# Kernel tuning notes

Measured on AMD Instinct MI355X. Metric: run time of the kernel, lower is better.

The kernel has to match this reference:

```python
import jax, jax.numpy as jnp
import numpy as np

MARGIN = 0.2
NEG_INF = -1e9  # safe stand-in for -inf when masking the max


def setup_inputs() -> dict:
    key = jax.random.key(0)
    k1, k2, k3 = jax.random.split(key, 3)
    B, D = 8192, 256
    p = jax.random.normal(k1, (B, D), dtype=jnp.float32)
    # module docstring says projections are normalized
    projections = p / jnp.linalg.norm(p, axis=1, keepdims=True)
    affordance_ids = jax.random.randint(k2, (B,), 0, 36, dtype=jnp.int64)
    instance_ids = jax.random.randint(k3, (B,), 0, 2048, dtype=jnp.int64)
    return {
        "projections": projections,
        "affordance_ids": affordance_ids,
        "instance_ids": instance_ids,
    }


def reference(projections, affordance_ids, instance_ids):
    # (B, B) cosine similarities
    sim = jnp.matmul(projections, projections.T)

    aff_eq = affordance_ids[:, None] == affordance_ids[None, :]
    inst_eq = instance_ids[:, None] == instance_ids[None, :]
    pos_mask = aff_eq & ~inst_eq          # same affordance, different instance
    neg_mask = ~aff_eq                    # different affordance

    # per-row hard negative: max similarity over negatives
    hard_neg = jnp.max(jnp.where(neg_mask, sim, NEG_INF), axis=1)  # (B,)

    # rows contribute only if they have >=1 positive AND >=1 negative
    valid_row = pos_mask.any(axis=1) & neg_mask.any(axis=1)        # (B,)
    pair_mask = pos_mask & valid_row[:, None]                      # (B, B)

    # margin loss for every (anchor i, positive j) pair
    losses = jnp.maximum(hard_neg[:, None] - sim + MARGIN, 0.0)

    total = jnp.sum(jnp.where(pair_mask, losses, 0.0))
    num_pairs = jnp.sum(pair_mask)
    return jnp.where(num_pairs > 0, total / num_pairs, 0.0)
```

## Files before the change

kernel.cpp:

```cpp
#include <hip/hip_runtime.h>

#define NB 8192
#define ND 256
#define NCLS 64
#define LOSS_MARGIN 0.2f
#define NEG_INF_F (-1e9f)
#define LMAXT 3
#define NBLK_LOSS (NCLS * LMAXT * LMAXT)
#define NTILE_T 2080

typedef __attribute__((ext_vector_type(8))) __bf16 bf16x8;
typedef __attribute__((ext_vector_type(4))) float f32x4;

__device__ __forceinline__ unsigned short f2bf(float f) {
  unsigned u = __float_as_uint(f);
  unsigned r = (u + 0x7fffu + ((u >> 16) & 1u)) >> 16;
  return (unsigned short)r;
}

__device__ __forceinline__ void gl_lds16(const void* gsrc, void* ldst) {
  __builtin_amdgcn_global_load_lds(
      (const __attribute__((address_space(1))) void*)gsrc,
      (__attribute__((address_space(3))) void*)ldst, 16, 0, 0);
}

__global__ __launch_bounds__(1024) void build_idx_fused(const int* __restrict__ aff,
                                                        int* __restrict__ class_start,
                                                        int* __restrict__ class_idx) {
  const int c = blockIdx.x;
  const int t = threadIdx.x;
  const int lane = t & 63, wave = t >> 6;
  __shared__ int wtot[16];
  __shared__ int s_off;

  int lt = 0;
  for (int i = t; i < NB; i += 1024) lt += (aff[i] < c) ? 1 : 0;
  for (int off = 32; off; off >>= 1) lt += __shfl_down(lt, off);
  if (lane == 0) wtot[wave] = lt;
  __syncthreads();
  int base = 0;
  for (int w = 0; w < 16; ++w) base += wtot[w];
  if (t == 0) {
    class_start[c] = base;
    if (c == 0) class_start[NCLS] = NB;
  }
  __syncthreads();
  if (t == 0) s_off = 0;
  __syncthreads();

  for (int pass = 0; pass < NB / 1024; ++pass) {
    const int i = pass * 1024 + t;
    const bool m = (aff[i] == c);
    const unsigned long long mask = __ballot(m);
    if (lane == 0) wtot[wave] = __popcll(mask);
    __syncthreads();
    const int off = s_off;
    int prefix = 0;
    for (int w = 0; w < wave; ++w) prefix += wtot[w];
    if (m)
      class_idx[base + off + prefix +
                __popcll(mask & ((1ull << lane) - 1ull))] = i;
    __syncthreads();
    if (t == 0) {
      int tot = 0;
      for (int w = 0; w < 16; ++w) tot += wtot[w];
      s_off = off + tot;
    }
    __syncthreads();
  }
}

__global__ __launch_bounds__(256) void gather_convert(const float* __restrict__ P,
                                                      const int* __restrict__ aff,
                                                      const int* __restrict__ inst,
                                                      const int* __restrict__ class_idx,
                                                      unsigned short* __restrict__ Psort,
                                                      int* __restrict__ affSort,
                                                      int* __restrict__ instSort) {
  const int t = threadIdx.x;
  const int sr = blockIdx.x * 8 + (t >> 5);
  const int c = t & 31;
  const int src = class_idx[sr];
  const float4* ps = (const float4*)(P + (size_t)src * ND);
  ushort4* pd = (ushort4*)(Psort + (size_t)sr * ND);
#pragma unroll
  for (int q = 0; q < 2; ++q) {
    float4 v = ps[c + q * 32];
    ushort4 h;
    h.x = f2bf(v.x); h.y = f2bf(v.y); h.z = f2bf(v.z); h.w = f2bf(v.w);
    pd[c + q * 32] = h;
  }
  if (c == 0) {
    affSort[sr] = aff[src];
    instSort[sr] = inst[src];
  }
}

__global__ __launch_bounds__(256, 4) void simmax_mfma(const unsigned short* __restrict__ Psort,
                                                      const int* __restrict__ affSort,
                                                      float* __restrict__ part) {
  int wg = blockIdx.x;
  wg = (wg & 7) * (NTILE_T / 8) + (wg >> 3);
  int bi = (int)((129.0f - sqrtf(129.0f * 129.0f - 8.0f * (float)wg)) * 0.5f);
  while (bi * 64 - bi * (bi - 1) / 2 > wg) --bi;
  while ((bi + 1) * 64 - (bi + 1) * bi / 2 <= wg) ++bi;
  const int bj = bi + (wg - (bi * 64 - bi * (bi - 1) / 2));

  __shared__ __align__(16) unsigned short At[2][4096];
  __shared__ __align__(16) unsigned short Bt[2][4096];
  __shared__ int affI[128], affJ[128];
  __shared__ float rowmax_s[128][2];
  __shared__ float colmax_s[128][2];

  const int t = threadIdx.x;
  const int lane = t & 63;
  const int wave = t >> 6;
  const int r0 = bi * 128, c0 = bj * 128;

  if (t < 128) affI[t] = affSort[r0 + t];
  else affJ[t - 128] = affSort[c0 + (t - 128)];

  const int wr = (wave >> 1) * 64;
  const int wc = (wave & 1) * 64;

  f32x4 acc[4][4];
#pragma unroll
  for (int m = 0; m < 4; ++m)
#pragma unroll
    for (int n = 0; n < 4; ++n) acc[m][n] = (f32x4){0.f, 0.f, 0.f, 0.f};

  const int ci0 = t, ci1 = 256 + t;
  const int kg0 = ci0 >> 7, rw0 = ci0 & 127;
  const int kg1 = ci1 >> 7, rw1 = ci1 & 127;

#define STAGE_SIM(B, KC)                                                      \
  do {                                                                        \
    gl_lds16(Psort + (size_t)(r0 + rw0) * ND + (KC) + kg0 * 8, &At[B][ci0 * 8]); \
    gl_lds16(Psort + (size_t)(c0 + rw0) * ND + (KC) + kg0 * 8, &Bt[B][ci0 * 8]); \
    gl_lds16(Psort + (size_t)(r0 + rw1) * ND + (KC) + kg1 * 8, &At[B][ci1 * 8]); \
    gl_lds16(Psort + (size_t)(c0 + rw1) * ND + (KC) + kg1 * 8, &Bt[B][ci1 * 8]); \
  } while (0)

  STAGE_SIM(0, 0);
  asm volatile("s_waitcnt vmcnt(0) lgkmcnt(0)" ::: "memory");
  __builtin_amdgcn_s_barrier();
  __builtin_amdgcn_sched_barrier(0);

  int cur = 0;
#pragma unroll 1
  for (int s = 0; s < 8; ++s) {
    if (s < 7) STAGE_SIM(cur ^ 1, (s + 1) * 32);
    const int kg = lane >> 4, lr = lane & 15;
    bf16x8 a[4], b[4];
#pragma unroll
    for (int m = 0; m < 4; ++m)
      a[m] = *(const bf16x8*)&At[cur][(kg * 128 + wr + m * 16 + lr) * 8];
#pragma unroll
    for (int n = 0; n < 4; ++n)
      b[n] = *(const bf16x8*)&Bt[cur][(kg * 128 + wc + n * 16 + lr) * 8];
#pragma unroll
    for (int m = 0; m < 4; ++m)
#pragma unroll
      for (int n = 0; n < 4; ++n)
        acc[m][n] = __builtin_amdgcn_mfma_f32_16x16x32_bf16(a[m], b[n], acc[m][n], 0, 0, 0);
    __builtin_amdgcn_sched_barrier(0);
    if (s < 7) {
      asm volatile("s_waitcnt vmcnt(0) lgkmcnt(0)" ::: "memory");
      __builtin_amdgcn_s_barrier();
      __builtin_amdgcn_sched_barrier(0);
    }
    cur ^= 1;
  }

#pragma unroll
  for (int m = 0; m < 4; ++m) {
#pragma unroll
    for (int r = 0; r < 4; ++r) {
      const int lrow = wr + m * 16 + (lane >> 4) * 4 + r;
      const int ai = affI[lrow];
      float rmax = NEG_INF_F;
#pragma unroll
      for (int n = 0; n < 4; ++n) {
        const int lcol = wc + n * 16 + (lane & 15);
        if (affJ[lcol] != ai) rmax = fmaxf(rmax, acc[m][n][r]);
      }
      rmax = fmaxf(rmax, __shfl_xor(rmax, 1));
      rmax = fmaxf(rmax, __shfl_xor(rmax, 2));
      rmax = fmaxf(rmax, __shfl_xor(rmax, 4));
      rmax = fmaxf(rmax, __shfl_xor(rmax, 8));
      if ((lane & 15) == 0) rowmax_s[lrow][wc >> 6] = rmax;
    }
  }
  if (bi != bj) {
#pragma unroll
    for (int n = 0; n < 4; ++n) {
      const int lcol = wc + n * 16 + (lane & 15);
      const int aj = affJ[lcol];
      float cmax = NEG_INF_F;
#pragma unroll
      for (int m = 0; m < 4; ++m) {
        const int lrb = wr + m * 16 + (lane >> 4) * 4;
#pragma unroll
        for (int r = 0; r < 4; ++r)
          if (affI[lrb + r] != aj) cmax = fmaxf(cmax, acc[m][n][r]);
      }
      cmax = fmaxf(cmax, __shfl_xor(cmax, 16));
      cmax = fmaxf(cmax, __shfl_xor(cmax, 32));
      if (lane < 16) colmax_s[lcol][wr >> 6] = cmax;
    }
  }
  __syncthreads();
  if (t < 128) {
    part[(size_t)(r0 + t) * 64 + bj] = fmaxf(rowmax_s[t][0], rowmax_s[t][1]);
  } else if (bi != bj) {
    const int c = t - 128;
    part[(size_t)(c0 + c) * 64 + bi] = fmaxf(colmax_s[c][0], colmax_s[c][1]);
  }
#undef STAGE_SIM
}

__global__ __launch_bounds__(256) void hn_reduce(const float* __restrict__ part,
                                                 float* __restrict__ hn) {
  const int i = blockIdx.x * 256 + threadIdx.x;
  const float4* p = (const float4*)(part + (size_t)i * 64);
  float m = NEG_INF_F;
#pragma unroll
  for (int q = 0; q < 16; ++q) {
    float4 v = p[q];
    m = fmaxf(m, fmaxf(fmaxf(v.x, v.y), fmaxf(v.z, v.w)));
  }
  hn[i] = m;
}

__global__ __launch_bounds__(256, 4) void loss_mfma(const unsigned short* __restrict__ Psort,
                                                    const int* __restrict__ class_start,
                                                    const int* __restrict__ instSort,
                                                    const float* __restrict__ hn,
                                                    float* __restrict__ bsum,
                                                    int* __restrict__ bcnt) {
  const int c = blockIdx.z;
  const int ti = blockIdx.x, tj = blockIdx.y;
  const int bid = (c * LMAXT + ti) * LMAXT + tj;
  const int t = threadIdx.x;
  const int base = class_start[c];
  const int cnt = class_start[c + 1] - base;
  const int nt = (cnt + 127) >> 7;
  if (ti >= nt || tj >= nt || cnt >= NB) {
    if (t == 0) { bsum[bid] = 0.f; bcnt[bid] = 0; }
    return;
  }

  __shared__ __align__(16) unsigned short At[2][4096];
  __shared__ __align__(16) unsigned short Bt[2][4096];
  __shared__ int instI[128], instJ[128];
  __shared__ float hnI[128];

  const int lane = t & 63;
  const int wave = t >> 6;

  if (t < 128) {
    int ri = ti * 128 + t;
    int gi = base + (ri < cnt ? ri : 0);
    instI[t] = instSort[gi];
    hnI[t] = hn[gi];
  } else {
    int tt = t - 128;
    int rj = tj * 128 + tt;
    int gj = base + (rj < cnt ? rj : 0);
    instJ[tt] = instSort[gj];
  }

  const int wr = (wave >> 1) * 64;
  const int wc = (wave & 1) * 64;

  f32x4 acc[4][4];
#pragma unroll
  for (int m = 0; m < 4; ++m)
#pragma unroll
    for (int n = 0; n < 4; ++n) acc[m][n] = (f32x4){0.f, 0.f, 0.f, 0.f};

  const int ci0 = t, ci1 = 256 + t;
  const int kg0 = ci0 >> 7, rw0 = ci0 & 127;
  const int kg1 = ci1 >> 7, rw1 = ci1 & 127;
  const int ra0 = base + (ti * 128 + rw0 < cnt ? ti * 128 + rw0 : 0);
  const int ra1 = base + (ti * 128 + rw1 < cnt ? ti * 128 + rw1 : 0);
  const int rb0 = base + (tj * 128 + rw0 < cnt ? tj * 128 + rw0 : 0);
  const int rb1 = base + (tj * 128 + rw1 < cnt ? tj * 128 + rw1 : 0);

#define STAGE_LOSS(B, KC)                                               \
  do {                                                                  \
    gl_lds16(Psort + (size_t)ra0 * ND + (KC) + kg0 * 8, &At[B][ci0 * 8]); \
    gl_lds16(Psort + (size_t)rb0 * ND + (KC) + kg0 * 8, &Bt[B][ci0 * 8]); \
    gl_lds16(Psort + (size_t)ra1 * ND + (KC) + kg1 * 8, &At[B][ci1 * 8]); \
    gl_lds16(Psort + (size_t)rb1 * ND + (KC) + kg1 * 8, &Bt[B][ci1 * 8]); \
  } while (0)

  STAGE_LOSS(0, 0);
  asm volatile("s_waitcnt vmcnt(0) lgkmcnt(0)" ::: "memory");
  __builtin_amdgcn_s_barrier();
  __builtin_amdgcn_sched_barrier(0);

  int cur = 0;
#pragma unroll 1
  for (int s = 0; s < 8; ++s) {
    if (s < 7) STAGE_LOSS(cur ^ 1, (s + 1) * 32);
    const int kg = lane >> 4, lr = lane & 15;
    bf16x8 a[4], b[4];
#pragma unroll
    for (int m = 0; m < 4; ++m)
      a[m] = *(const bf16x8*)&At[cur][(kg * 128 + wr + m * 16 + lr) * 8];
#pragma unroll
    for (int n = 0; n < 4; ++n)
      b[n] = *(const bf16x8*)&Bt[cur][(kg * 128 + wc + n * 16 + lr) * 8];
#pragma unroll
    for (int m = 0; m < 4; ++m)
#pragma unroll
      for (int n = 0; n < 4; ++n)
        acc[m][n] = __builtin_amdgcn_mfma_f32_16x16x32_bf16(a[m], b[n], acc[m][n], 0, 0, 0);
    __builtin_amdgcn_sched_barrier(0);
    if (s < 7) {
      asm volatile("s_waitcnt vmcnt(0) lgkmcnt(0)" ::: "memory");
      __builtin_amdgcn_s_barrier();
      __builtin_amdgcn_sched_barrier(0);
    }
    cur ^= 1;
  }

  float lsum = 0.f;
  int lcnt = 0;
#pragma unroll
  for (int m = 0; m < 4; ++m) {
#pragma unroll
    for (int r = 0; r < 4; ++r) {
      const int lrow = wr + m * 16 + (lane >> 4) * 4 + r;
      const int ri = ti * 128 + lrow;
      if (ri >= cnt) continue;
      const float hnv = hnI[lrow];
      const int ii = instI[lrow];
#pragma unroll
      for (int n = 0; n < 4; ++n) {
        const int lcol = wc + n * 16 + (lane & 15);
        const int rj = tj * 128 + lcol;
        if (rj < cnt && instJ[lcol] != ii) {
          lsum += fmaxf(hnv - acc[m][n][r] + LOSS_MARGIN, 0.f);
          lcnt += 1;
        }
      }
    }
  }

  for (int off = 32; off; off >>= 1) {
    lsum += __shfl_down(lsum, off);
    lcnt += __shfl_down(lcnt, off);
  }
  __shared__ float wsum[4];
  __shared__ int wcnt[4];
  if (lane == 0) { wsum[wave] = lsum; wcnt[wave] = lcnt; }
  __syncthreads();
  if (t == 0) {
    bsum[bid] = wsum[0] + wsum[1] + wsum[2] + wsum[3];
    bcnt[bid] = wcnt[0] + wcnt[1] + wcnt[2] + wcnt[3];
  }
#undef STAGE_LOSS
}

__global__ __launch_bounds__(256) void finalize_kernel(const float* __restrict__ bsum,
                                                       const int* __restrict__ bcnt,
                                                       float* __restrict__ out) {
  const int t = threadIdx.x;
  float s = 0.f;
  int n = 0;
  for (int i = t; i < NBLK_LOSS; i += 256) { s += bsum[i]; n += bcnt[i]; }
  for (int off = 32; off; off >>= 1) {
    s += __shfl_down(s, off);
    n += __shfl_down(n, off);
  }
  __shared__ float wsum[4];
  __shared__ int wcnt[4];
  if ((t & 63) == 0) { wsum[t >> 6] = s; wcnt[t >> 6] = n; }
  __syncthreads();
  if (t == 0) {
    const float S = wsum[0] + wsum[1] + wsum[2] + wsum[3];
    const int N = wcnt[0] + wcnt[1] + wcnt[2] + wcnt[3];
    out[0] = (N > 0) ? (S / (float)N) : 0.0f;
  }
}

extern "C" void kernel_launch(void* const* d_in, const int* in_sizes, int n_in,
                              void* d_out, int out_size, void* d_ws, size_t ws_size,
                              hipStream_t stream) {
  const float* P = (const float*)d_in[0];
  const int* aff = (const int*)d_in[1];
  const int* inst = (const int*)d_in[2];
  float* out = (float*)d_out;

  unsigned short* Psort = (unsigned short*)d_ws;
  float* part = (float*)((char*)d_ws + (size_t)NB * ND * 2);
  int* ibase = (int*)((char*)part + (size_t)NB * 64 * 4);
  float* hn        = (float*)ibase;
  int* class_start = ibase + NB;
  int* class_idx   = ibase + NB + NCLS + 1;
  int* affSort     = ibase + 2 * NB + NCLS + 1;
  int* instSort    = ibase + 3 * NB + NCLS + 1;
  float* bsum = (float*)(ibase + 4 * NB + NCLS + 1);
  int* bcnt   = ibase + 4 * NB + NCLS + 1 + NBLK_LOSS;

  build_idx_fused<<<NCLS, 1024, 0, stream>>>(aff, class_start, class_idx);
  gather_convert<<<NB / 8, 256, 0, stream>>>(P, aff, inst, class_idx, Psort,
                                             affSort, instSort);
  simmax_mfma<<<NTILE_T, 256, 0, stream>>>(Psort, affSort, part);
  hn_reduce<<<NB / 256, 256, 0, stream>>>(part, hn);
  loss_mfma<<<dim3(LMAXT, LMAXT, NCLS), 256, 0, stream>>>(Psort, class_start, instSort,
                                                          hn, bsum, bcnt);
  finalize_kernel<<<1, 256, 0, stream>>>(bsum, bcnt, out);
}
```

Baseline: 90.62 us.

## Triple-buffer LDS staging with partial vmcnt waits in both MFMA kernels

Result: no change. 92.22 us (+1.8%).

```diff
diff --git a/kernel.cpp b/kernel.cpp
--- a/kernel.cpp
+++ b/kernel.cpp
@@ -96,7 +96,7 @@
   }
 }
 
-__global__ __launch_bounds__(256, 4) void simmax_mfma(const unsigned short* __restrict__ Psort,
+__global__ __launch_bounds__(256, 3) void simmax_mfma(const unsigned short* __restrict__ Psort,
                                                       const int* __restrict__ affSort,
                                                       float* __restrict__ part) {
   int wg = blockIdx.x;
@@ -106,8 +106,8 @@
   while ((bi + 1) * 64 - (bi + 1) * bi / 2 <= wg) ++bi;
   const int bj = bi + (wg - (bi * 64 - bi * (bi - 1) / 2));
 
-  __shared__ __align__(16) unsigned short At[2][4096];
-  __shared__ __align__(16) unsigned short Bt[2][4096];
+  __shared__ __align__(16) unsigned short At[3][4096];
+  __shared__ __align__(16) unsigned short Bt[3][4096];
   __shared__ int affI[128], affJ[128];
   __shared__ float rowmax_s[128][2];
   __shared__ float colmax_s[128][2];
@@ -141,36 +141,46 @@
     gl_lds16(Psort + (size_t)(c0 + rw1) * ND + (KC) + kg1 * 8, &Bt[B][ci1 * 8]); \
   } while (0)
 
+#define KSTEP_SIM(S, VM)                                                      \
+  do {                                                                        \
+    asm volatile("s_waitcnt vmcnt(" #VM ")" ::: "memory");                    \
+    __builtin_amdgcn_s_barrier();                                             \
+    __builtin_amdgcn_sched_barrier(0);                                        \
+    const int kg = lane >> 4, lr = lane & 15;                                 \
+    bf16x8 a[4], b[4];                                                        \
+    _Pragma("unroll")                                                         \
+    for (int m = 0; m < 4; ++m)                                               \
+      a[m] = *(const bf16x8*)&At[(S) % 3][(kg * 128 + wr + m * 16 + lr) * 8]; \
+    _Pragma("unroll")                                                         \
+    for (int n = 0; n < 4; ++n)                                               \
+      b[n] = *(const bf16x8*)&Bt[(S) % 3][(kg * 128 + wc + n * 16 + lr) * 8]; \
+    __builtin_amdgcn_s_setprio(1);                                            \
+    _Pragma("unroll")                                                         \
+    for (int m = 0; m < 4; ++m)                                               \
+      _Pragma("unroll")                                                       \
+      for (int n = 0; n < 4; ++n)                                             \
+        acc[m][n] = __builtin_amdgcn_mfma_f32_16x16x32_bf16(a[m], b[n], acc[m][n], 0, 0, 0); \
+    __builtin_amdgcn_s_setprio(0);                                            \
+    __builtin_amdgcn_sched_barrier(0);                                        \
+    if ((S) < 5) {                                                            \
+      __builtin_amdgcn_s_barrier();                                           \
+      __builtin_amdgcn_sched_barrier(0);                                      \
+      STAGE_SIM((S) % 3, ((S) + 3) * 32);                                     \
+    }                                                                         \
+  } while (0)
+
   STAGE_SIM(0, 0);
-  asm volatile("s_waitcnt vmcnt(0) lgkmcnt(0)" ::: "memory");
-  __builtin_amdgcn_s_barrier();
-  __builtin_amdgcn_sched_barrier(0);
-
-  int cur = 0;
-#pragma unroll 1
-  for (int s = 0; s < 8; ++s) {
-    if (s < 7) STAGE_SIM(cur ^ 1, (s + 1) * 32);
-    const int kg = lane >> 4, lr = lane & 15;
-    bf16x8 a[4], b[4];
-#pragma unroll
-    for (int m = 0; m < 4; ++m)
-      a[m] = *(const bf16x8*)&At[cur][(kg * 128 + wr + m * 16 + lr) * 8];
-#pragma unroll
-    for (int n = 0; n < 4; ++n)
-      b[n] = *(const bf16x8*)&Bt[cur][(kg * 128 + wc + n * 16 + lr) * 8];
-#pragma unroll
-    for (int m = 0; m < 4; ++m)
-#pragma unroll
-      for (int n = 0; n < 4; ++n)
-        acc[m][n] = __builtin_amdgcn_mfma_f32_16x16x32_bf16(a[m], b[n], acc[m][n], 0, 0, 0);
-    __builtin_amdgcn_sched_barrier(0);
-    if (s < 7) {
-      asm volatile("s_waitcnt vmcnt(0) lgkmcnt(0)" ::: "memory");
-      __builtin_amdgcn_s_barrier();
-      __builtin_amdgcn_sched_barrier(0);
-    }
-    cur ^= 1;
-  }
+  STAGE_SIM(1, 32);
+  STAGE_SIM(2, 64);
+
+  KSTEP_SIM(0, 8);
+  KSTEP_SIM(1, 8);
+  KSTEP_SIM(2, 8);
+  KSTEP_SIM(3, 8);
+  KSTEP_SIM(4, 8);
+  KSTEP_SIM(5, 8);
+  KSTEP_SIM(6, 4);
+  KSTEP_SIM(7, 0);
 
 #pragma unroll
   for (int m = 0; m < 4; ++m) {
@@ -216,6 +226,7 @@
     const int c = t - 128;
     part[(size_t)(c0 + c) * 64 + bi] = fmaxf(colmax_s[c][0], colmax_s[c][1]);
   }
+#undef KSTEP_SIM
 #undef STAGE_SIM
 }
 
@@ -232,7 +243,7 @@
   hn[i] = m;
 }
 
-__global__ __launch_bounds__(256, 4) void loss_mfma(const unsigned short* __restrict__ Psort,
+__global__ __launch_bounds__(256, 3) void loss_mfma(const unsigned short* __restrict__ Psort,
                                                     const int* __restrict__ class_start,
                                                     const int* __restrict__ instSort,
                                                     const float* __restrict__ hn,
@@ -250,8 +261,8 @@
     return;
   }
 
-  __shared__ __align__(16) unsigned short At[2][4096];
-  __shared__ __align__(16) unsigned short Bt[2][4096];
+  __shared__ __align__(16) unsigned short At[3][4096];
+  __shared__ __align__(16) unsigned short Bt[3][4096];
   __shared__ int instI[128], instJ[128];
   __shared__ float hnI[128];
 
@@ -295,36 +306,46 @@
     gl_lds16(Psort + (size_t)rb1 * ND + (KC) + kg1 * 8, &Bt[B][ci1 * 8]); \
   } while (0)
 
+#define KSTEP_LOSS(S, VM)                                                     \
+  do {                                                                        \
+    asm volatile("s_waitcnt vmcnt(" #VM ")" ::: "memory");                    \
+    __builtin_amdgcn_s_barrier();                                             \
+    __builtin_amdgcn_sched_barrier(0);                                        \
+    const int kg = lane >> 4, lr = lane & 15;                                 \
+    bf16x8 a[4], b[4];                                                        \
+    _Pragma("unroll")                                                         \
+    for (int m = 0; m < 4; ++m)                                               \
+      a[m] = *(const bf16x8*)&At[(S) % 3][(kg * 128 + wr + m * 16 + lr) * 8]; \
+    _Pragma("unroll")                                                         \
+    for (int n = 0; n < 4; ++n)                                               \
+      b[n] = *(const bf16x8*)&Bt[(S) % 3][(kg * 128 + wc + n * 16 + lr) * 8]; \
+    __builtin_amdgcn_s_setprio(1);                                            \
+    _Pragma("unroll")                                                         \
+    for (int m = 0; m < 4; ++m)                                               \
+      _Pragma("unroll")                                                       \
+      for (int n = 0; n < 4; ++n)                                             \
+        acc[m][n] = __builtin_amdgcn_mfma_f32_16x16x32_bf16(a[m], b[n], acc[m][n], 0, 0, 0); \
+    __builtin_amdgcn_s_setprio(0);                                            \
+    __builtin_amdgcn_sched_barrier(0);                                        \
+    if ((S) < 5) {                                                            \
+      __builtin_amdgcn_s_barrier();                                           \
+      __builtin_amdgcn_sched_barrier(0);                                      \
+      STAGE_LOSS((S) % 3, ((S) + 3) * 32);                                    \
+    }                                                                         \
+  } while (0)
+
   STAGE_LOSS(0, 0);
-  asm volatile("s_waitcnt vmcnt(0) lgkmcnt(0)" ::: "memory");
-  __builtin_amdgcn_s_barrier();
-  __builtin_amdgcn_sched_barrier(0);
-
-  int cur = 0;
-#pragma unroll 1
-  for (int s = 0; s < 8; ++s) {
-    if (s < 7) STAGE_LOSS(cur ^ 1, (s + 1) * 32);
-    const int kg = lane >> 4, lr = lane & 15;
-    bf16x8 a[4], b[4];
-#pragma unroll
-    for (int m = 0; m < 4; ++m)
-      a[m] = *(const bf16x8*)&At[cur][(kg * 128 + wr + m * 16 + lr) * 8];
-#pragma unroll
-    for (int n = 0; n < 4; ++n)
-      b[n] = *(const bf16x8*)&Bt[cur][(kg * 128 + wc + n * 16 + lr) * 8];
-#pragma unroll
-    for (int m = 0; m < 4; ++m)
-#pragma unroll
-      for (int n = 0; n < 4; ++n)
-        acc[m][n] = __builtin_amdgcn_mfma_f32_16x16x32_bf16(a[m], b[n], acc[m][n], 0, 0, 0);
-    __builtin_amdgcn_sched_barrier(0);
-    if (s < 7) {
-      asm volatile("s_waitcnt vmcnt(0) lgkmcnt(0)" ::: "memory");
-      __builtin_amdgcn_s_barrier();
-      __builtin_amdgcn_sched_barrier(0);
-    }
-    cur ^= 1;
-  }
+  STAGE_LOSS(1, 32);
+  STAGE_LOSS(2, 64);
+
+  KSTEP_LOSS(0, 8);
+  KSTEP_LOSS(1, 8);
+  KSTEP_LOSS(2, 8);
+  KSTEP_LOSS(3, 8);
+  KSTEP_LOSS(4, 8);
+  KSTEP_LOSS(5, 8);
+  KSTEP_LOSS(6, 4);
+  KSTEP_LOSS(7, 0);
 
   float lsum = 0.f;
   int lcnt = 0;
@@ -361,6 +382,7 @@
     bsum[bid] = wsum[0] + wsum[1] + wsum[2] + wsum[3];
     bcnt[bid] = wcnt[0] + wcnt[1] + wcnt[2] + wcnt[3];
   }
+#undef KSTEP_LOSS
 #undef STAGE_LOSS
 }
 
```

## Fuse index build with gather, fold hn reduce into loss, skip masks

Applied to the files above, without the earlier changes.

After: 99.11 us. 1.09x slower.

```diff
diff --git a/kernel.cpp b/kernel.cpp
--- a/kernel.cpp
+++ b/kernel.cpp
@@ -8,6 +8,7 @@
 #define LMAXT 3
 #define NBLK_LOSS (NCLS * LMAXT * LMAXT)
 #define NTILE_T 2080
+#define MAXCLS 640
 
 typedef __attribute__((ext_vector_type(8))) __bf16 bf16x8;
 typedef __attribute__((ext_vector_type(4))) float f32x4;
@@ -24,14 +25,19 @@
       (__attribute__((address_space(3))) void*)ldst, 16, 0, 0);
 }
 
-__global__ __launch_bounds__(1024) void build_idx_fused(const int* __restrict__ aff,
-                                                        int* __restrict__ class_start,
-                                                        int* __restrict__ class_idx) {
+__global__ __launch_bounds__(1024) void prep_kernel(const float* __restrict__ P,
+                                                    const int* __restrict__ aff,
+                                                    const int* __restrict__ inst,
+                                                    int* __restrict__ class_start,
+                                                    unsigned short* __restrict__ Psort,
+                                                    int* __restrict__ affSort,
+                                                    int* __restrict__ instSort) {
   const int c = blockIdx.x;
   const int t = threadIdx.x;
   const int lane = t & 63, wave = t >> 6;
   __shared__ int wtot[16];
   __shared__ int s_off;
+  __shared__ int lds_idx[MAXCLS];
 
   int lt = 0;
   for (int i = t; i < NB; i += 1024) lt += (aff[i] < c) ? 1 : 0;
@@ -57,9 +63,10 @@
     const int off = s_off;
     int prefix = 0;
     for (int w = 0; w < wave; ++w) prefix += wtot[w];
-    if (m)
-      class_idx[base + off + prefix +
-                __popcll(mask & ((1ull << lane) - 1ull))] = i;
+    if (m) {
+      int pos = off + prefix + __popcll(mask & ((1ull << lane) - 1ull));
+      if (pos < MAXCLS) lds_idx[pos] = i;
+    }
     __syncthreads();
     if (t == 0) {
       int tot = 0;
@@ -68,31 +75,19 @@
     }
     __syncthreads();
   }
-}
-
-__global__ __launch_bounds__(256) void gather_convert(const float* __restrict__ P,
-                                                      const int* __restrict__ aff,
-                                                      const int* __restrict__ inst,
-                                                      const int* __restrict__ class_idx,
-                                                      unsigned short* __restrict__ Psort,
-                                                      int* __restrict__ affSort,
-                                                      int* __restrict__ instSort) {
-  const int t = threadIdx.x;
-  const int sr = blockIdx.x * 8 + (t >> 5);
-  const int c = t & 31;
-  const int src = class_idx[sr];
-  const float4* ps = (const float4*)(P + (size_t)src * ND);
-  ushort4* pd = (ushort4*)(Psort + (size_t)sr * ND);
-#pragma unroll
-  for (int q = 0; q < 2; ++q) {
-    float4 v = ps[c + q * 32];
+  const int cnt = s_off;
+
+  for (int k = wave; k < cnt; k += 16) {
+    const int src = lds_idx[k];
+    const int sr = base + k;
+    const float4 v = ((const float4*)(P + (size_t)src * ND))[lane];
     ushort4 h;
     h.x = f2bf(v.x); h.y = f2bf(v.y); h.z = f2bf(v.z); h.w = f2bf(v.w);
-    pd[c + q * 32] = h;
-  }
-  if (c == 0) {
-    affSort[sr] = aff[src];
-    instSort[sr] = inst[src];
+    ((ushort4*)(Psort + (size_t)sr * ND))[lane] = h;
+    if (lane == 0) {
+      affSort[sr] = c;
+      instSort[sr] = inst[src];
+    }
   }
 }
 
@@ -117,8 +112,11 @@
   const int wave = t >> 6;
   const int r0 = bi * 128, c0 = bj * 128;
 
-  if (t < 128) affI[t] = affSort[r0 + t];
-  else affJ[t - 128] = affSort[c0 + (t - 128)];
+  const bool needMask = (affSort[c0] <= affSort[r0 + 127]);
+  if (needMask) {
+    if (t < 128) affI[t] = affSort[r0 + t];
+    else affJ[t - 128] = affSort[c0 + (t - 128)];
+  }
 
   const int wr = (wave >> 1) * 64;
   const int wc = (wave & 1) * 64;
@@ -165,77 +163,92 @@
         acc[m][n] = __builtin_amdgcn_mfma_f32_16x16x32_bf16(a[m], b[n], acc[m][n], 0, 0, 0);
     __builtin_amdgcn_sched_barrier(0);
     if (s < 7) {
-      asm volatile("s_waitcnt vmcnt(0) lgkmcnt(0)" ::: "memory");
+      asm volatile("s_waitcnt vmcnt(0)" ::: "memory");
       __builtin_amdgcn_s_barrier();
       __builtin_amdgcn_sched_barrier(0);
     }
     cur ^= 1;
   }
 
-#pragma unroll
-  for (int m = 0; m < 4; ++m) {
-#pragma unroll
-    for (int r = 0; r < 4; ++r) {
-      const int lrow = wr + m * 16 + (lane >> 4) * 4 + r;
-      const int ai = affI[lrow];
-      float rmax = NEG_INF_F;
+  if (needMask) {
+#pragma unroll
+    for (int m = 0; m < 4; ++m) {
+#pragma unroll
+      for (int r = 0; r < 4; ++r) {
+        const int lrow = wr + m * 16 + (lane >> 4) * 4 + r;
+        const int ai = affI[lrow];
+        float rmax = NEG_INF_F;
+#pragma unroll
+        for (int n = 0; n < 4; ++n) {
+          const int lcol = wc + n * 16 + (lane & 15);
+          if (affJ[lcol] != ai) rmax = fmaxf(rmax, acc[m][n][r]);
+        }
+        rmax = fmaxf(rmax, __shfl_xor(rmax, 1));
+        rmax = fmaxf(rmax, __shfl_xor(rmax, 2));
+        rmax = fmaxf(rmax, __shfl_xor(rmax, 4));
+        rmax = fmaxf(rmax, __shfl_xor(rmax, 8));
+        if ((lane & 15) == 0) rowmax_s[lrow][wc >> 6] = rmax;
+      }
+    }
+    if (bi != bj) {
 #pragma unroll
       for (int n = 0; n < 4; ++n) {
         const int lcol = wc + n * 16 + (lane & 15);
-        if (affJ[lcol] != ai) rmax = fmaxf(rmax, acc[m][n][r]);
+        const int aj = affJ[lcol];
+        float cmax = NEG_INF_F;
+#pragma unroll
+        for (int m = 0; m < 4; ++m) {
+          const int lrb = wr + m * 16 + (lane >> 4) * 4;
+#pragma unroll
+          for (int r = 0; r < 4; ++r)
+            if (affI[lrb + r] != aj) cmax = fmaxf(cmax, acc[m][n][r]);
+        }
+        cmax = fmaxf(cmax, __shfl_xor(cmax, 16));
+        cmax = fmaxf(cmax, __shfl_xor(cmax, 32));
+        if (lane < 16) colmax_s[lcol][wr >> 6] = cmax;
       }
-      rmax = fmaxf(rmax, __shfl_xor(rmax, 1));
-      rmax = fmaxf(rmax, __shfl_xor(rmax, 2));
-      rmax = fmaxf(rmax, __shfl_xor(rmax, 4));
-      rmax = fmaxf(rmax, __shfl_xor(rmax, 8));
-      if ((lane & 15) == 0) rowmax_s[lrow][wc >> 6] = rmax;
-    }
-  }
-  if (bi != bj) {
+    }
+  } else {
+#pragma unroll
+    for (int m = 0; m < 4; ++m) {
+#pragma unroll
+      for (int r = 0; r < 4; ++r) {
+        float rmax = fmaxf(fmaxf(acc[m][0][r], acc[m][1][r]),
+                           fmaxf(acc[m][2][r], acc[m][3][r]));
+        rmax = fmaxf(rmax, __shfl_xor(rmax, 1));
+        rmax = fmaxf(rmax, __shfl_xor(rmax, 2));
+        rmax = fmaxf(rmax, __shfl_xor(rmax, 4));
+        rmax = fmaxf(rmax, __shfl_xor(rmax, 8));
+        if ((lane & 15) == 0)
+          rowmax_s[wr + m * 16 + (lane >> 4) * 4 + r][wc >> 6] = rmax;
+      }
+    }
 #pragma unroll
     for (int n = 0; n < 4; ++n) {
-      const int lcol = wc + n * 16 + (lane & 15);
-      const int aj = affJ[lcol];
       float cmax = NEG_INF_F;
 #pragma unroll
-      for (int m = 0; m < 4; ++m) {
-        const int lrb = wr + m * 16 + (lane >> 4) * 4;
-#pragma unroll
-        for (int r = 0; r < 4; ++r)
-          if (affI[lrb + r] != aj) cmax = fmaxf(cmax, acc[m][n][r]);
-      }
+      for (int m = 0; m < 4; ++m)
+#pragma unroll
+        for (int r = 0; r < 4; ++r) cmax = fmaxf(cmax, acc[m][n][r]);
       cmax = fmaxf(cmax, __shfl_xor(cmax, 16));
       cmax = fmaxf(cmax, __shfl_xor(cmax, 32));
-      if (lane < 16) colmax_s[lcol][wr >> 6] = cmax;
+      if (lane < 16) colmax_s[wc + n * 16 + (lane & 15)][wr >> 6] = cmax;
     }
   }
   __syncthreads();
   if (t < 128) {
-    part[(size_t)(r0 + t) * 64 + bj] = fmaxf(rowmax_s[t][0], rowmax_s[t][1]);
+    part[(size_t)bj * NB + (r0 + t)] = fmaxf(rowmax_s[t][0], rowmax_s[t][1]);
   } else if (bi != bj) {
-    const int c = t - 128;
-    part[(size_t)(c0 + c) * 64 + bi] = fmaxf(colmax_s[c][0], colmax_s[c][1]);
+    const int cc = t - 128;
+    part[(size_t)bi * NB + (c0 + cc)] = fmaxf(colmax_s[cc][0], colmax_s[cc][1]);
   }
 #undef STAGE_SIM
-}
-
-__global__ __launch_bounds__(256) void hn_reduce(const float* __restrict__ part,
-                                                 float* __restrict__ hn) {
-  const int i = blockIdx.x * 256 + threadIdx.x;
-  const float4* p = (const float4*)(part + (size_t)i * 64);
-  float m = NEG_INF_F;
-#pragma unroll
-  for (int q = 0; q < 16; ++q) {
-    float4 v = p[q];
-    m = fmaxf(m, fmaxf(fmaxf(v.x, v.y), fmaxf(v.z, v.w)));
-  }
-  hn[i] = m;
 }
 
 __global__ __launch_bounds__(256, 4) void loss_mfma(const unsigned short* __restrict__ Psort,
                                                     const int* __restrict__ class_start,
                                                     const int* __restrict__ instSort,
-                                                    const float* __restrict__ hn,
+                                                    const float* __restrict__ part,
                                                     float* __restrict__ bsum,
                                                     int* __restrict__ bcnt) {
   const int c = blockIdx.z;
@@ -262,7 +275,10 @@
     int ri = ti * 128 + t;
     int gi = base + (ri < cnt ? ri : 0);
     instI[t] = instSort[gi];
-    hnI[t] = hn[gi];
+    float m = NEG_INF_F;
+#pragma unroll 16
+    for (int q = 0; q < 64; ++q) m = fmaxf(m, part[(size_t)q * NB + gi]);
+    hnI[t] = m;
   } else {
     int tt = t - 128;
     int rj = tj * 128 + tt;
@@ -319,7 +335,7 @@
         acc[m][n] = __builtin_amdgcn_mfma_f32_16x16x32_bf16(a[m], b[n], acc[m][n], 0, 0, 0);
     __builtin_amdgcn_sched_barrier(0);
     if (s < 7) {
-      asm volatile("s_waitcnt vmcnt(0) lgkmcnt(0)" ::: "memory");
+      asm volatile("s_waitcnt vmcnt(0)" ::: "memory");
       __builtin_amdgcn_s_barrier();
       __builtin_amdgcn_sched_barrier(0);
     }
@@ -396,21 +412,17 @@
 
   unsigned short* Psort = (unsigned short*)d_ws;
   float* part = (float*)((char*)d_ws + (size_t)NB * ND * 2);
-  int* ibase = (int*)((char*)part + (size_t)NB * 64 * 4);
-  float* hn        = (float*)ibase;
-  int* class_start = ibase + NB;
-  int* class_idx   = ibase + NB + NCLS + 1;
-  int* affSort     = ibase + 2 * NB + NCLS + 1;
-  int* instSort    = ibase + 3 * NB + NCLS + 1;
-  float* bsum = (float*)(ibase + 4 * NB + NCLS + 1);
-  int* bcnt   = ibase + 4 * NB + NCLS + 1 + NBLK_LOSS;
-
-  build_idx_fused<<<NCLS, 1024, 0, stream>>>(aff, class_start, class_idx);
-  gather_convert<<<NB / 8, 256, 0, stream>>>(P, aff, inst, class_idx, Psort,
-                                             affSort, instSort);
+  int* ibase = (int*)((char*)part + (size_t)64 * NB * 4);
+  int* class_start = ibase;
+  int* affSort     = ibase + NCLS + 1;
+  int* instSort    = ibase + NCLS + 1 + NB;
+  float* bsum = (float*)(ibase + NCLS + 1 + 2 * NB);
+  int* bcnt   = ibase + NCLS + 1 + 2 * NB + NBLK_LOSS;
+
+  prep_kernel<<<NCLS, 1024, 0, stream>>>(P, aff, inst, class_start, Psort,
+                                         affSort, instSort);
   simmax_mfma<<<NTILE_T, 256, 0, stream>>>(Psort, affSort, part);
-  hn_reduce<<<NB / 256, 256, 0, stream>>>(part, hn);
   loss_mfma<<<dim3(LMAXT, LMAXT, NCLS), 256, 0, stream>>>(Psort, class_start, instSort,
-                                                          hn, bsum, bcnt);
+                                                          part, bsum, bcnt);
   finalize_kernel<<<1, 256, 0, stream>>>(bsum, bcnt, out);
 }
```
